# Kernel optimization log

Hardware: AMD Instinct MI355X
Metric: run time of the kernel (lower is better)

## Reference

```python
import jax, jax.numpy as jnp
import numpy as np

NUM_HEADS = 16
EMBED_DIM = 1024
HEAD_DIM = EMBED_DIM // NUM_HEADS
SCALE = HEAD_DIM * -0.5  # faithful to source: multiplicative, negative


def setup_inputs() -> dict:
    key = jax.random.key(0)
    kx, kq, kk, kv, ko = jax.random.split(key, 5)
    B, S, E = 2, 2048, EMBED_DIM
    std = 1.0 / np.sqrt(E)
    return {
        "x": jax.random.normal(kx, (B, S, E), dtype=jnp.float32),
        "Wq": jax.random.normal(kq, (E, E), dtype=jnp.float32) * std,
        "Wk": jax.random.normal(kk, (E, E), dtype=jnp.float32) * std,
        "Wv": jax.random.normal(kv, (E, E), dtype=jnp.float32) * std,
        "Wo": jax.random.normal(ko, (E, E), dtype=jnp.float32) * std,
    }


def reference(x, Wq, Wk, Wv, Wo):
    B, S, E = x.shape
    H, D = NUM_HEADS, HEAD_DIM
    # nn.Linear(bias=False): y = x @ W.T
    q = (x @ Wq.T).reshape(B, S, H, D).transpose(0, 2, 1, 3)  # unused downstream (faithful to source)
    k = (x @ Wk.T).reshape(B, S, H, D).transpose(0, 2, 1, 3)  # [B,H,S,D]
    v = (x @ Wv.T).reshape(B, S, H, D).transpose(0, 2, 1, 3)
    # Source bug reproduced: logits = K @ V^T, scaled by head_dim * -0.5
    logits = jnp.einsum('bhsd,bhtd->bhst', k, v) * SCALE  # [B,H,S,S]
    attn = jax.nn.softmax(logits, axis=-1)
    out = jnp.einsum('bhst,bhtd->bhsd', attn, v)  # [B,H,S,D]
    out = out.transpose(0, 2, 1, 3).reshape(B, S, E)
    return out @ Wo.T
```

## Files before the change

kernel.cpp:

```cpp
#include <hip/hip_runtime.h>
#include <math.h>

#define B_ 2
#define S_ 2048
#define E_ 1024
#define H_ 16
#define D_ 64
#define M_ (B_ * S_)
#define SC2 (-46.166241308446828f)

typedef unsigned short u16;
typedef _Float16 f16;
typedef __attribute__((ext_vector_type(8))) _Float16 f16x8;
typedef __attribute__((ext_vector_type(2))) __fp16 fp16x2_n;
typedef __attribute__((ext_vector_type(16))) float f32x16;

static __device__ __forceinline__ f32x16 mfma_h(f16x8 a, f16x8 b, f32x16 c) {
    return __builtin_amdgcn_mfma_f32_32x32x16_f16(a, b, c, 0, 0, 0);
}
static __device__ __forceinline__ u16 f16bits(f16 h) {
    union { f16 h; u16 u; } c; c.h = h; return c.u;
}
static __device__ __forceinline__ unsigned pack2(u16 a, u16 b) {
    return (unsigned)a | ((unsigned)b << 16);
}
static __device__ __forceinline__ unsigned pkrtz(float a, float b) {
    fp16x2_n h = __builtin_amdgcn_cvt_pkrtz(a, b);
    unsigned u; __builtin_memcpy(&u, &h, 4); return u;
}
static __device__ __forceinline__ void pl32swap(unsigned &a, unsigned &b) {
    asm volatile("v_permlane32_swap_b32 %0, %1" : "+v"(a), "+v"(b));
}
static __device__ __forceinline__ void lgkm_bar() {
    asm volatile("s_waitcnt lgkmcnt(0)" ::: "memory");
    __builtin_amdgcn_s_barrier();
}
#define ROWMAP(r, hh) (((r) & 3) + ((((r) >> 2)) << 3) + ((hh) << 2))

__global__ __launch_bounds__(256)
void convert_split(const float* __restrict__ x, const float* __restrict__ Wk,
                   const float* __restrict__ Wv, const float* __restrict__ Wo,
                   u16* __restrict__ Xh, u16* __restrict__ Xl,
                   u16* __restrict__ Wkh, u16* __restrict__ Wkl,
                   u16* __restrict__ Wvh, u16* __restrict__ Wvl,
                   u16* __restrict__ Woh)
{
    const int blk = blockIdx.x;
    const float* src; u16 *dh, *dl; int base; float sc = 1.0f; bool wantlo = true;
    if (blk < 4096)      { src = x;  dh = Xh;  dl = Xl;  base = blk; }
    else if (blk < 5120) { src = Wk; dh = Wkh; dl = Wkl; base = blk - 4096; sc = SC2; }
    else if (blk < 6144) { src = Wv; dh = Wvh; dl = Wvl; base = blk - 5120; }
    else                 { src = Wo; dh = Woh; dl = Woh; base = blk - 6144; wantlo = false; }
    const size_t off = ((size_t)base * 256 + threadIdx.x) * 4;
    const float4 v = *(const float4*)(src + off);
    const float f[4] = {v.x * sc, v.y * sc, v.z * sc, v.w * sc};
    u16 h4[4], l4[4];
#pragma unroll
    for (int i = 0; i < 4; ++i) {
        const f16 h = (f16)f[i];
        h4[i] = f16bits(h);
        l4[i] = f16bits((f16)(f[i] - (float)h));
    }
    *(uint2*)(dh + off) = make_uint2(pack2(h4[0], h4[1]), pack2(h4[2], h4[3]));
    if (wantlo)
        *(uint2*)(dl + off) = make_uint2(pack2(l4[0], l4[1]), pack2(l4[2], l4[3]));
}

#define CSB 1032

template<int MODE>
__global__ __launch_bounds__(1024, 4)
void gemm_f(const u16* __restrict__ Ah_, const u16* __restrict__ Al_,
            const u16* __restrict__ Bkh_, const u16* __restrict__ Bkl_,
            const u16* __restrict__ Bvh_, const u16* __restrict__ Bvl_,
            u16* __restrict__ Khg, u16* __restrict__ Klg,
            u16* __restrict__ Vhg, u16* __restrict__ Vtg,
            float* __restrict__ Cout)
{
    constexpr int BK   = (MODE == 0 ? 64 : 128);
    constexpr int NCH  = BK / 8;
    constexpr int NKK  = NCH / 4;
    constexpr int ARRX = NCH * CSB;
    constexpr int NIT  = E_ / BK;
    extern __shared__ u16 stage[];

    const int tid = threadIdx.x;
    const int w = tid >> 6, l31 = tid & 31, hh = (tid >> 5) & 1;
    const int wt = w & 7, ws = w >> 3;
    const int wm = (wt >> 1) << 5, wn = (wt & 1) << 6;
    const int m0 = blockIdx.y * 128, n0 = blockIdx.x * 128;
    const int ch8 = (ws << 1) + hh;

    const int sr = tid >> 3, sch = tid & 7;
    const size_t gA = (size_t)(m0 + sr) * E_ + (sch << 3);
    const size_t gB = (size_t)(n0 + sr) * E_ + (sch << 3);
    const int slo = sch * CSB + sr * 8;

    f32x16 acc1[2], acc2[2];
#pragma unroll
    for (int nt = 0; nt < 2; ++nt)
#pragma unroll
        for (int r = 0; r < 16; ++r) {
            acc1[nt][r] = 0.f;
            if constexpr (MODE == 0) acc2[nt][r] = 0.f;
        }

    constexpr int NPF = (MODE == 0 ? 6 : 4);
    f16x8 pf0[NPF], pf1[NPF];
    auto load_tile = [&](int k0, f16x8* pf) {
        if constexpr (MODE == 0) {
            pf[0] = *(const f16x8*)(Ah_ + gA + k0);
            pf[1] = *(const f16x8*)(Al_ + gA + k0);
            pf[2] = *(const f16x8*)(Bkh_ + gB + k0);
            pf[3] = *(const f16x8*)(Bkl_ + gB + k0);
            pf[4] = *(const f16x8*)(Bvh_ + gB + k0);
            pf[5] = *(const f16x8*)(Bvl_ + gB + k0);
        } else {
            pf[0] = *(const f16x8*)(Ah_ + gA + k0);
            pf[1] = *(const f16x8*)(Ah_ + gA + k0 + 64);
            pf[2] = *(const f16x8*)(Bkh_ + gB + k0);
            pf[3] = *(const f16x8*)(Bkh_ + gB + k0 + 64);
        }
    };
    auto store_tile = [&](int bb, f16x8* pf) {
        if constexpr (MODE == 0) {
#pragma unroll
            for (int a = 0; a < 6; ++a)
                *(f16x8*)&stage[bb + a * ARRX + slo] = pf[a];
        } else {
            *(f16x8*)&stage[bb + slo] = pf[0];
            *(f16x8*)&stage[bb + (sch + 8) * CSB + sr * 8] = pf[1];
            *(f16x8*)&stage[bb + ARRX + slo] = pf[2];
            *(f16x8*)&stage[bb + ARRX + (sch + 8) * CSB + sr * 8] = pf[3];
        }
    };
    auto compute = [&](int bb) {
#pragma unroll
        for (int kk = 0; kk < NKK; ++kk) {
            const int co = bb + (ch8 + (kk << 2)) * CSB;
            const int offx = co + (wm + l31) * 8;
            const f16x8 xh = *(const f16x8*)&stage[0 * ARRX + offx];
            f16x8 xl;
            if constexpr (MODE == 0) xl = *(const f16x8*)&stage[1 * ARRX + offx];
#pragma unroll
            for (int nt = 0; nt < 2; ++nt) {
                const int ro = co + (wn + (nt << 5) + l31) * 8;
                if constexpr (MODE == 0) {
                    const f16x8 bkh = *(const f16x8*)&stage[2 * ARRX + ro];
                    const f16x8 bkl = *(const f16x8*)&stage[3 * ARRX + ro];
                    const f16x8 bvh = *(const f16x8*)&stage[4 * ARRX + ro];
                    const f16x8 bvl = *(const f16x8*)&stage[5 * ARRX + ro];
                    acc1[nt] = mfma_h(xh, bkh, acc1[nt]);
                    acc1[nt] = mfma_h(xh, bkl, acc1[nt]);
                    acc1[nt] = mfma_h(xl, bkh, acc1[nt]);
                    acc2[nt] = mfma_h(xh, bvh, acc2[nt]);
                    acc2[nt] = mfma_h(xh, bvl, acc2[nt]);
                    acc2[nt] = mfma_h(xl, bvh, acc2[nt]);
                } else {
                    const f16x8 bh = *(const f16x8*)&stage[ARRX + ro];
                    acc1[nt] = mfma_h(xh, bh, acc1[nt]);
                }
            }
        }
    };

    if constexpr (MODE == 0) {
        load_tile(0, pf0);
        for (int it = 0; it < NIT; ++it) {
            store_tile(0, pf0);
            lgkm_bar();
            if (it + 1 < NIT) load_tile((it + 1) * BK, pf0);
            compute(0);
            lgkm_bar();
        }
    } else {
        load_tile(0, pf0);
        store_tile(0, pf0);
        load_tile(BK, pf1);
        lgkm_bar();
        for (int p = 0; p < NIT / 2; ++p) {
            const int e = 2 * p;
            if (e + 2 < NIT) load_tile((e + 2) * BK, pf0);
            compute(0);
            store_tile(2 * ARRX, pf1);
            lgkm_bar();
            if (e + 3 < NIT) load_tile((e + 3) * BK, pf1);
            compute(2 * ARRX);
            if (e + 2 < NIT) store_tile(0, pf0);
            lgkm_bar();
        }
    }

    float* red = (float*)stage;
    constexpr int NR = (MODE == 0 ? 4 : 2);
#pragma unroll
    for (int rd = 0; rd < NR; ++rd) {
        const int ntr = rd & 1;
        f32x16* A = (MODE == 0 && rd >= 2) ? &acc2[ntr] : &acc1[ntr];
        __syncthreads();
        if (ws == 1) {
#pragma unroll
            for (int r = 0; r < 16; ++r)
                red[(wt << 10) + (r << 6) + (hh << 5) + l31] = (*A)[r];
        }
        __syncthreads();
        if (ws == 0) {
#pragma unroll
            for (int r = 0; r < 16; ++r)
                (*A)[r] += red[(wt << 10) + (r << 6) + (hh << 5) + l31];
        }
    }
    if (ws != 0) return;

#pragma unroll
    for (int nt = 0; nt < 2; ++nt) {
        const int n = n0 + wn + (nt << 5) + l31;
        if constexpr (MODE == 1) {
#pragma unroll
            for (int r = 0; r < 16; ++r) {
                const int m = m0 + wm + ROWMAP(r, hh);
                Cout[(size_t)m * E_ + n] = acc1[nt][r];
            }
        } else {
            const int hd = n >> 6, d = n & 63;
            const int b = m0 >> 11;
            u16 vb16[16];
#pragma unroll
            for (int r = 0; r < 16; ++r) {
                const int s = (m0 + wm + ROWMAP(r, hh)) & (S_ - 1);
                const size_t ib = (((size_t)(b * H_ + hd) << 11) + s) * D_ + d;
                const float kv = acc1[nt][r];
                const f16 kh = (f16)kv;
                Khg[ib] = f16bits(kh);
                Klg[ib] = f16bits((f16)(kv - (float)kh));
                const f16 vh = (f16)acc2[nt][r];
                vb16[r] = f16bits(vh);
                Vhg[ib] = vb16[r];
            }
            const size_t vtb = ((size_t)(b * H_ + hd) * D_ + d) << 11;
#pragma unroll
            for (int g = 0; g < 4; ++g) {
                const int s0 = ((m0 + wm) & (S_ - 1)) + (g << 3) + (hh << 2);
                *(uint2*)&Vtg[vtb + s0] =
                    make_uint2(pack2(vb16[4 * g], vb16[4 * g + 1]),
                               pack2(vb16[4 * g + 2], vb16[4 * g + 3]));
            }
        }
    }
}

#define CSA 520
#define VA  (8 * CSA)

__global__ __launch_bounds__(512, 2)
void attn_mfma(const u16* __restrict__ Kh, const u16* __restrict__ Kl,
               const u16* __restrict__ Vh, const u16* __restrict__ Vt,
               u16* __restrict__ Obuf)
{
    __shared__ u16 sV[4 * VA];

    const int tid = threadIdx.x;
    const int w = tid >> 6, l31 = tid & 31, hh = (tid >> 5) & 1;
    const int bh = blockIdx.y;
    const int sbase = blockIdx.x * 256 + (w << 5);
    const int sg = sbase + l31;

    f16x8 kfh[4], kfl[4];
    {
        const size_t kb = ((size_t)bh * S_ + sg) * D_;
#pragma unroll
        for (int ks = 0; ks < 4; ++ks) {
            const int db = (ks << 4) + (hh << 3);
            kfh[ks] = *(const f16x8*)(Kh + kb + db);
            kfl[ks] = *(const f16x8*)(Kl + kb + db);
        }
    }

    f32x16 oacc[2];
#pragma unroll
    for (int r = 0; r < 16; ++r) { oacc[0][r] = 0.f; oacc[1][r] = 0.f; }
    float m_i = -INFINITY, l_i = 0.f;

    const int rr = tid >> 3, cc = tid & 7;
    const size_t gn = ((size_t)bh * S_ + rr) * D_ + (cc << 3);
    const size_t gt = ((size_t)bh * D_ + rr) * S_ + (cc << 3);
    const int slo = cc * CSA + rr * 8;

    f16x8 pv[2];
    auto load_tile = [&](int it2) {
        const size_t t0 = (size_t)it2 << 6;
        pv[0] = *(const f16x8*)(Vh + gn + t0 * D_);
        pv[1] = *(const f16x8*)(Vt + gt + t0);
    };

    load_tile(0);
    *(f16x8*)&sV[slo] = pv[0];
    *(f16x8*)&sV[VA + slo] = pv[1];
    __syncthreads();

    for (int it = 0; it < 32; ++it) {
        const int vb = (it & 1) * (2 * VA);
        const int nb = ((it + 1) & 1) * (2 * VA);
        if (it + 1 < 32) load_tile(it + 1);

        f32x16 sta[2], stb[2];
#pragma unroll
        for (int r = 0; r < 16; ++r) {
            sta[0][r] = 0.f; sta[1][r] = 0.f;
            stb[0][r] = 0.f; stb[1][r] = 0.f;
        }
#pragma unroll
        for (int ks = 0; ks < 4; ++ks) {
            const int ch = (ks << 1) + hh;
#pragma unroll
            for (int mt = 0; mt < 2; ++mt) {
                const f16x8 av = *(const f16x8*)&sV[vb + ch * CSA + ((mt << 5) + l31) * 8];
                sta[mt] = mfma_h(av, kfh[ks], sta[mt]);
                stb[mt] = mfma_h(av, kfl[ks], stb[mt]);
            }
        }
#pragma unroll
        for (int mt = 0; mt < 2; ++mt)
#pragma unroll
            for (int r = 0; r < 16; ++r) sta[mt][r] += stb[mt][r];

        float tmax = -INFINITY;
#pragma unroll
        for (int mt = 0; mt < 2; ++mt)
#pragma unroll
            for (int r = 0; r < 16; ++r) tmax = fmaxf(tmax, sta[mt][r]);
        tmax = fmaxf(tmax, __shfl_xor(tmax, 32));
        const float mnew = fmaxf(m_i, tmax);
        const float alpha = __builtin_amdgcn_exp2f(m_i - mnew);
        m_i = mnew;
        const unsigned long long cmask = __ballot(tmax >= mnew - 30.f);

        if (cmask) {
            float rsum = 0.f;
#pragma unroll
            for (int mt = 0; mt < 2; ++mt)
#pragma unroll
                for (int r = 0; r < 16; ++r) {
                    const float p = __builtin_amdgcn_exp2f(sta[mt][r] - mnew);
                    sta[mt][r] = p;
                    rsum += p;
                }
            rsum += __shfl_xor(rsum, 32);
            l_i = l_i * alpha + rsum;

#pragma unroll
            for (int r = 0; r < 16; ++r) { oacc[0][r] *= alpha; oacc[1][r] *= alpha; }

            unsigned pa[2][4], pb[2][4];
#pragma unroll
            for (int mt = 0; mt < 2; ++mt)
#pragma unroll
                for (int q = 0; q < 4; ++q) {
                    pa[mt][q] = pkrtz(sta[mt][4 * q + 0], sta[mt][4 * q + 1]);
                    pb[mt][q] = pkrtz(sta[mt][4 * q + 2], sta[mt][4 * q + 3]);
                }

#pragma unroll
            for (int ks = 0; ks < 4; ++ks) {
                const int mt = ks >> 1, kk = ks & 1;
                unsigned w0 = pa[mt][2 * kk], w2v = pa[mt][2 * kk + 1];
                pl32swap(w0, w2v);
                unsigned w1 = pb[mt][2 * kk], w3v = pb[mt][2 * kk + 1];
                pl32swap(w1, w3v);
                union { unsigned u[4]; f16x8 v; } bw;
                bw.u[0] = w0; bw.u[1] = w1; bw.u[2] = w2v; bw.u[3] = w3v;
                const int ch = (ks << 1) + hh;
#pragma unroll
                for (int nt = 0; nt < 2; ++nt) {
                    const f16x8 vtf = *(const f16x8*)&sV[vb + VA + ch * CSA + ((nt << 5) + l31) * 8];
                    oacc[nt] = mfma_h(vtf, bw.v, oacc[nt]);
                }
            }
        }

        if (it + 1 < 32) {
            *(f16x8*)&sV[nb + slo] = pv[0];
            *(f16x8*)&sV[nb + VA + slo] = pv[1];
        }
        __syncthreads();
    }

    const float linv = (l_i > 0.f) ? (1.0f / l_i) : 0.f;
    const int b = bh >> 4;
    const int hd = bh & 15;
    u16* Or = Obuf + ((size_t)b * S_ + sg) * E_ + (hd << 6);
#pragma unroll
    for (int nt = 0; nt < 2; ++nt)
#pragma unroll
        for (int q = 0; q < 4; ++q) {
            const int d0 = (nt << 5) + (q << 3) + (hh << 2);
            u16 c[4];
#pragma unroll
            for (int j = 0; j < 4; ++j)
                c[j] = f16bits((f16)(oacc[nt][4 * q + j] * linv));
            *(uint2*)&Or[d0] = make_uint2(pack2(c[0], c[1]), pack2(c[2], c[3]));
        }
}

extern "C" void kernel_launch(void* const* d_in, const int* in_sizes, int n_in,
                              void* d_out, int out_size, void* d_ws, size_t ws_size,
                              hipStream_t stream)
{
    (void)in_sizes; (void)n_in; (void)out_size; (void)ws_size;
    const float* x  = (const float*)d_in[0];
    const float* Wk = (const float*)d_in[2];
    const float* Wv = (const float*)d_in[3];
    const float* Wo = (const float*)d_in[4];
    float* out = (float*)d_out;

    char* ws = (char*)d_ws;
    const size_t MB = 1u << 20;
    u16* Xh  = (u16*)(ws + 0 * MB);
    u16* Xl  = (u16*)(ws + 8 * MB);
    u16* Wkh = (u16*)(ws + 16 * MB);
    u16* Wkl = (u16*)(ws + 18 * MB);
    u16* Wvh = (u16*)(ws + 20 * MB);
    u16* Wvl = (u16*)(ws + 22 * MB);
    u16* Woh = (u16*)(ws + 24 * MB);
    u16* Kh  = (u16*)(ws + 26 * MB);
    u16* Kl  = (u16*)(ws + 34 * MB);
    u16* Vh  = (u16*)(ws + 42 * MB);
    u16* Vt  = (u16*)(ws + 50 * MB);
    u16* Obuf = Xl;

    const int lds0 = 6 * (8 * CSB) * (int)sizeof(u16);
    const int lds1 = 2 * 2 * (16 * CSB) * (int)sizeof(u16);
    static bool attr_done = false;
    if (!attr_done) {
        hipFuncSetAttribute(reinterpret_cast<const void*>(&gemm_f<0>),
                            hipFuncAttributeMaxDynamicSharedMemorySize, lds0);
        hipFuncSetAttribute(reinterpret_cast<const void*>(&gemm_f<1>),
                            hipFuncAttributeMaxDynamicSharedMemorySize, lds1);
        attr_done = true;
    }

    convert_split<<<7168, 256, 0, stream>>>(x, Wk, Wv, Wo,
                                            Xh, Xl, Wkh, Wkl, Wvh, Wvl, Woh);
    gemm_f<0><<<dim3(E_ / 128, M_ / 128), 1024, lds0, stream>>>(
        Xh, Xl, Wkh, Wkl, Wvh, Wvl, Kh, Kl, Vh, Vt, nullptr);
    attn_mfma<<<dim3(S_ / 256, B_ * H_), 512, 0, stream>>>(Kh, Kl, Vh, Vt, Obuf);
    gemm_f<1><<<dim3(E_ / 128, M_ / 128), 1024, lds1, stream>>>(
        Obuf, Obuf, Woh, Woh, Woh, Woh,
        nullptr, nullptr, nullptr, nullptr, out);
}
```

Baseline: 219.5 us.

## Load A operand directly to registers and double-buffer B tiles in QKV GEMM

In the fused K/V projection GEMM, each wave now loads its X hi/lo fragments straight from global memory into registers instead of staging them through LDS. This frees LDS space, which is used to double-buffer the four weight arrays so the next tile's store overlaps compute, reusing the ping-pong schedule of the output GEMM. It also removes one LDS write and read per A element. The cost is redundant global reads of A across waves that share rows, and more registers held for prefetch.

```diff
diff --git a/kernel.cpp b/kernel.cpp
--- a/kernel.cpp
+++ b/kernel.cpp
@@ -81,6 +81,8 @@
     constexpr int NCH  = BK / 8;
     constexpr int NKK  = NCH / 4;
     constexpr int ARRX = NCH * CSB;
+    constexpr int NARR = (MODE == 0 ? 4 : 2);
+    constexpr int BUFS = NARR * ARRX;
     constexpr int NIT  = E_ / BK;
     extern __shared__ u16 stage[];
 
@@ -95,6 +97,7 @@
     const size_t gA = (size_t)(m0 + sr) * E_ + (sch << 3);
     const size_t gB = (size_t)(n0 + sr) * E_ + (sch << 3);
     const int slo = sch * CSB + sr * 8;
+    const size_t aRow = (size_t)(m0 + wm + l31) * E_;
 
     f32x16 acc1[2], acc2[2];
 #pragma unroll
@@ -105,16 +108,14 @@
             if constexpr (MODE == 0) acc2[nt][r] = 0.f;
         }
 
-    constexpr int NPF = (MODE == 0 ? 6 : 4);
-    f16x8 pf0[NPF], pf1[NPF];
+    f16x8 pf0[4], pf1[4];
+    f16x8 axA[4], axB[4];
     auto load_tile = [&](int k0, f16x8* pf) {
         if constexpr (MODE == 0) {
-            pf[0] = *(const f16x8*)(Ah_ + gA + k0);
-            pf[1] = *(const f16x8*)(Al_ + gA + k0);
-            pf[2] = *(const f16x8*)(Bkh_ + gB + k0);
-            pf[3] = *(const f16x8*)(Bkl_ + gB + k0);
-            pf[4] = *(const f16x8*)(Bvh_ + gB + k0);
-            pf[5] = *(const f16x8*)(Bvl_ + gB + k0);
+            pf[0] = *(const f16x8*)(Bkh_ + gB + k0);
+            pf[1] = *(const f16x8*)(Bkl_ + gB + k0);
+            pf[2] = *(const f16x8*)(Bvh_ + gB + k0);
+            pf[3] = *(const f16x8*)(Bvl_ + gB + k0);
         } else {
             pf[0] = *(const f16x8*)(Ah_ + gA + k0);
             pf[1] = *(const f16x8*)(Ah_ + gA + k0 + 64);
@@ -122,10 +123,16 @@
             pf[3] = *(const f16x8*)(Bkh_ + gB + k0 + 64);
         }
     };
+    auto load_a = [&](int k0, f16x8* ax) {
+        ax[0] = *(const f16x8*)(Ah_ + aRow + k0 + (ch8 << 3));
+        ax[1] = *(const f16x8*)(Ah_ + aRow + k0 + ((ch8 + 4) << 3));
+        ax[2] = *(const f16x8*)(Al_ + aRow + k0 + (ch8 << 3));
+        ax[3] = *(const f16x8*)(Al_ + aRow + k0 + ((ch8 + 4) << 3));
+    };
     auto store_tile = [&](int bb, f16x8* pf) {
         if constexpr (MODE == 0) {
 #pragma unroll
-            for (int a = 0; a < 6; ++a)
+            for (int a = 0; a < 4; ++a)
                 *(f16x8*)&stage[bb + a * ARRX + slo] = pf[a];
         } else {
             *(f16x8*)&stage[bb + slo] = pf[0];
@@ -134,61 +141,67 @@
             *(f16x8*)&stage[bb + ARRX + (sch + 8) * CSB + sr * 8] = pf[3];
         }
     };
-    auto compute = [&](int bb) {
+    auto compute0 = [&](int bb, const f16x8* ax) {
+#pragma unroll
+        for (int kk = 0; kk < 2; ++kk) {
+            const int co = bb + (ch8 + (kk << 2)) * CSB;
+            const f16x8 xh = ax[kk], xl = ax[2 + kk];
+#pragma unroll
+            for (int nt = 0; nt < 2; ++nt) {
+                const int rb = co + (wn + (nt << 5) + l31) * 8;
+                const f16x8 bkh = *(const f16x8*)&stage[rb + 0 * ARRX];
+                const f16x8 bkl = *(const f16x8*)&stage[rb + 1 * ARRX];
+                const f16x8 bvh = *(const f16x8*)&stage[rb + 2 * ARRX];
+                const f16x8 bvl = *(const f16x8*)&stage[rb + 3 * ARRX];
+                acc1[nt] = mfma_h(xh, bkh, acc1[nt]);
+                acc1[nt] = mfma_h(xh, bkl, acc1[nt]);
+                acc1[nt] = mfma_h(xl, bkh, acc1[nt]);
+                acc2[nt] = mfma_h(xh, bvh, acc2[nt]);
+                acc2[nt] = mfma_h(xh, bvl, acc2[nt]);
+                acc2[nt] = mfma_h(xl, bvh, acc2[nt]);
+            }
+        }
+    };
+    auto compute1 = [&](int bb) {
 #pragma unroll
         for (int kk = 0; kk < NKK; ++kk) {
             const int co = bb + (ch8 + (kk << 2)) * CSB;
-            const int offx = co + (wm + l31) * 8;
-            const f16x8 xh = *(const f16x8*)&stage[0 * ARRX + offx];
-            f16x8 xl;
-            if constexpr (MODE == 0) xl = *(const f16x8*)&stage[1 * ARRX + offx];
+            const f16x8 xh = *(const f16x8*)&stage[co + (wm + l31) * 8];
 #pragma unroll
             for (int nt = 0; nt < 2; ++nt) {
                 const int ro = co + (wn + (nt << 5) + l31) * 8;
-                if constexpr (MODE == 0) {
-                    const f16x8 bkh = *(const f16x8*)&stage[2 * ARRX + ro];
-                    const f16x8 bkl = *(const f16x8*)&stage[3 * ARRX + ro];
-                    const f16x8 bvh = *(const f16x8*)&stage[4 * ARRX + ro];
-                    const f16x8 bvl = *(const f16x8*)&stage[5 * ARRX + ro];
-                    acc1[nt] = mfma_h(xh, bkh, acc1[nt]);
-                    acc1[nt] = mfma_h(xh, bkl, acc1[nt]);
-                    acc1[nt] = mfma_h(xl, bkh, acc1[nt]);
-                    acc2[nt] = mfma_h(xh, bvh, acc2[nt]);
-                    acc2[nt] = mfma_h(xh, bvl, acc2[nt]);
-                    acc2[nt] = mfma_h(xl, bvh, acc2[nt]);
-                } else {
-                    const f16x8 bh = *(const f16x8*)&stage[ARRX + ro];
-                    acc1[nt] = mfma_h(xh, bh, acc1[nt]);
-                }
-            }
-        }
-    };
-
-    if constexpr (MODE == 0) {
-        load_tile(0, pf0);
-        for (int it = 0; it < NIT; ++it) {
-            store_tile(0, pf0);
-            lgkm_bar();
-            if (it + 1 < NIT) load_tile((it + 1) * BK, pf0);
-            compute(0);
-            lgkm_bar();
-        }
-    } else {
-        load_tile(0, pf0);
-        store_tile(0, pf0);
-        load_tile(BK, pf1);
+                const f16x8 bh = *(const f16x8*)&stage[ARRX + ro];
+                acc1[nt] = mfma_h(xh, bh, acc1[nt]);
+            }
+        }
+    };
+
+    load_tile(0, pf0);
+    if constexpr (MODE == 0) load_a(0, axA);
+    store_tile(0, pf0);
+    load_tile(BK, pf1);
+    if constexpr (MODE == 0) load_a(BK, axB);
+    lgkm_bar();
+    for (int p = 0; p < NIT / 2; ++p) {
+        const int e = 2 * p;
+        if (e + 2 < NIT) load_tile((e + 2) * BK, pf0);
+        if constexpr (MODE == 0) {
+            compute0(0, axA);
+            if (e + 2 < NIT) load_a((e + 2) * BK, axA);
+        } else {
+            compute1(0);
+        }
+        store_tile(BUFS, pf1);
         lgkm_bar();
-        for (int p = 0; p < NIT / 2; ++p) {
-            const int e = 2 * p;
-            if (e + 2 < NIT) load_tile((e + 2) * BK, pf0);
-            compute(0);
-            store_tile(2 * ARRX, pf1);
-            lgkm_bar();
-            if (e + 3 < NIT) load_tile((e + 3) * BK, pf1);
-            compute(2 * ARRX);
-            if (e + 2 < NIT) store_tile(0, pf0);
-            lgkm_bar();
-        }
+        if (e + 3 < NIT) load_tile((e + 3) * BK, pf1);
+        if constexpr (MODE == 0) {
+            compute0(BUFS, axB);
+            if (e + 3 < NIT) load_a((e + 3) * BK, axB);
+        } else {
+            compute1(BUFS);
+        }
+        if (e + 2 < NIT) store_tile(0, pf0);
+        lgkm_bar();
     }
 
     float* red = (float*)stage;
@@ -428,7 +441,7 @@
     u16* Vt  = (u16*)(ws + 50 * MB);
     u16* Obuf = Xl;
 
-    const int lds0 = 6 * (8 * CSB) * (int)sizeof(u16);
+    const int lds0 = 2 * 4 * (8 * CSB) * (int)sizeof(u16);
     const int lds1 = 2 * 2 * (16 * CSB) * (int)sizeof(u16);
     static bool attr_done = false;
     if (!attr_done) {
```

After: 275.6 us. +25.6%, slower.
